# Kernel tuning notes

Measured on AMD Instinct MI355X. Metric: run time of the kernel, lower is better.

The kernel has to match this reference:

```python
import math
import jax, jax.numpy as jnp
import numpy as np

DIM = 1024
HID = 2048  # dim * expansion_factor
QK = 128
G = 256  # group size
NUM_BUCKETS = 32
MAX_DIST = 128
SCALE = QK ** 0.5


def t5_rel_bias(rel_emb, g):
    # non-causal T5 relative position bias over a g x g window
    pos = jnp.arange(g)
    n = pos[:, None] - pos[None, :]  # n = -(k - q) = q - k
    nb = NUM_BUCKETS // 2  # 16
    ret = (n < 0).astype(jnp.int32) * nb
    n = jnp.abs(n)
    max_exact = nb // 2  # 8
    is_small = n < max_exact
    val_large = max_exact + (
        jnp.log(jnp.maximum(n, 1).astype(jnp.float32) / max_exact)
        / math.log(MAX_DIST / max_exact) * (nb - max_exact)
    ).astype(jnp.int32)
    val_large = jnp.minimum(val_large, nb - 1)
    bucket = ret + jnp.where(is_small, n, val_large)
    return rel_emb[bucket, 0] * SCALE  # [g, g]


def setup_inputs() -> dict:
    key = jax.random.key(0)
    ks = jax.random.split(key, 8)
    d = {}
    d['x'] = jax.random.normal(ks[0], (4, 4096, DIM), dtype=jnp.float32)
    d['ln_g'] = jnp.ones((DIM,), jnp.float32)
    d['ln_b'] = jnp.zeros((DIM,), jnp.float32)
    d['W_h'] = jax.random.normal(ks[1], (DIM, 2 * HID), jnp.float32) * (1.0 / math.sqrt(DIM))
    d['b_h'] = jnp.zeros((2 * HID,), jnp.float32)
    d['W_qk'] = jax.random.normal(ks[2], (DIM, QK), jnp.float32) * (1.0 / math.sqrt(DIM))
    d['b_qk'] = jnp.zeros((QK,), jnp.float32)
    d['os_g'] = 1.0 + 0.02 * jax.random.normal(ks[3], (4, QK), jnp.float32)
    d['os_b'] = jnp.zeros((4, QK), jnp.float32)
    d['rel_emb'] = jax.random.normal(ks[4], (NUM_BUCKETS, 1), jnp.float32)
    d['W_o'] = jax.random.normal(ks[5], (HID, DIM), jnp.float32) * (1.0 / math.sqrt(HID))
    d['b_o'] = jnp.zeros((DIM,), jnp.float32)
    return d


def reference(x, ln_g, ln_b, W_h, b_h, W_qk, b_qk, os_g, os_b, rel_emb, W_o, b_o):
    b, n, _ = x.shape
    # LayerNorm
    mu = jnp.mean(x, axis=-1, keepdims=True)
    var = jnp.var(x, axis=-1, keepdims=True)
    normed = (x - mu) * jax.lax.rsqrt(var + 1e-5) * ln_g + ln_b
    # to_hidden -> v, gate ; to_qk
    hidden = jax.nn.silu(normed @ W_h + b_h)  # [b, n, 2*HID]
    v, gate = hidden[..., :HID], hidden[..., HID:]
    qk = jax.nn.silu(normed @ W_qk + b_qk)  # [b, n, QK]
    # offset-scale into 4 heads
    heads = qk[..., None, :] * os_g + os_b  # [b, n, 4, QK]
    quad_q, lin_q, quad_k, lin_k = [heads[..., h, :] for h in range(4)]
    # group: n divisible by G (no padding needed)
    ng = n // G
    grp = lambda t: t.reshape(b, ng, G, -1)
    quad_q, quad_k, lin_q, lin_k, vg = map(grp, (quad_q, quad_k, lin_q, lin_k, v))
    # grouped quadratic attention with ReLU^2 and T5 bias
    sim = jnp.einsum('bgid,bgjd->bgij', quad_q, quad_k) / G
    sim = sim + t5_rel_bias(rel_emb, G)
    attn = jnp.square(jax.nn.relu(sim))
    quad_out = jnp.einsum('bgij,bgjd->bgid', attn, vg)
    # linear attention, reduced over groups (non-causal)
    lin_kv = jnp.einsum('bgnd,bgne->bde', lin_k, vg) / n
    lin_out = jnp.einsum('bgnd,bde->bgne', lin_q, lin_kv)
    out = gate * (quad_out.reshape(b, n, HID) + lin_out.reshape(b, n, HID))
    return out @ W_o + b_o + x
```

## Files before the change

### kernel.cpp

```cpp
#include <hip/hip_runtime.h>
#include <hip/hip_bf16.h>

typedef float  f32x4  __attribute__((ext_vector_type(4)));
typedef __bf16 bf16x8 __attribute__((ext_vector_type(8)));
typedef __bf16 bf16x4 __attribute__((ext_vector_type(4)));

__device__ __forceinline__ float silu_f(float x) { return x / (1.0f + __expf(-x)); }

__device__ __forceinline__ void gload16(const __bf16* g, const char* lds) {
    __builtin_amdgcn_global_load_lds((const __attribute__((address_space(1))) void*)g,
                                     (__attribute__((address_space(3))) void*)lds, 16, 0, 0);
}

__device__ __forceinline__ bf16x8 ds_read16(unsigned addr) {
    bf16x8 d;
    asm volatile("ds_read_b128 %0, %1" : "=v"(d) : "v"(addr));
    return d;
}

template<int IMB>
__device__ __forceinline__ void mfma16(f32x4 (&acc)[8][4], bf16x8 (&bA)[4], bf16x8 (&bB)[4]) {
#pragma unroll
    for (int im = 0; im < 4; ++im)
#pragma unroll
        for (int nj = 0; nj < 4; ++nj)
            acc[IMB + im][nj] = __builtin_amdgcn_mfma_f32_16x16x32_bf16(bA[im], bB[nj], acc[IMB + im][nj], 0, 0, 0);
}

__global__ __launch_bounds__(256) void ln_kernel(const float* __restrict__ x,
                                                 const float* __restrict__ g,
                                                 const float* __restrict__ b,
                                                 __bf16* __restrict__ out) {
    int row = blockIdx.x;
    const float* xr = x + (long)row * 1024;
    int t = threadIdx.x;
    f32x4 v = *(const f32x4*)(xr + t * 4);
    float s  = v[0] + v[1] + v[2] + v[3];
    float ss = v[0]*v[0] + v[1]*v[1] + v[2]*v[2] + v[3]*v[3];
    #pragma unroll
    for (int off = 32; off > 0; off >>= 1) {
        s  += __shfl_down(s, off);
        ss += __shfl_down(ss, off);
    }
    __shared__ float red[8];
    int wave = t >> 6, lane = t & 63;
    if (lane == 0) { red[wave*2] = s; red[wave*2+1] = ss; }
    __syncthreads();
    float S  = red[0] + red[2] + red[4] + red[6];
    float SS = red[1] + red[3] + red[5] + red[7];
    float mean = S * (1.0f/1024.0f);
    float var  = SS * (1.0f/1024.0f) - mean*mean;
    float rstd = rsqrtf(var + 1e-5f);
    __bf16* orow = out + (long)row * 1024;
    #pragma unroll
    for (int j = 0; j < 4; j++) {
        float fv = (v[j] - mean) * rstd * g[t*4+j] + b[t*4+j];
        orow[t*4+j] = (__bf16)fv;
    }
}

__global__ __launch_bounds__(256) void relbias_kernel(const float* __restrict__ rel_emb,
                                                      float* __restrict__ bmat) {
    int idx = blockIdx.x * 256 + threadIdx.x;
    int i = idx >> 8, j = idx & 255;
    int n = i - j;
    int ret = (n < 0) ? 16 : 0;
    int an = (n < 0) ? -n : n;
    int bucket;
    if (an < 8) {
        bucket = ret + an;
    } else {
        float vl = logf((float)an * 0.125f) / 2.772588722239781f * 8.0f;
        int lv = 8 + (int)vl;
        bucket = ret + (lv < 15 ? lv : 15);
    }
    bmat[idx] = rel_emb[bucket] * 11.313708498984761f;
}

__global__ __launch_bounds__(256) void transpose_kernel(const float* __restrict__ in,
                                                        __bf16* __restrict__ out,
                                                        int rows, int cols) {
    __shared__ __bf16 tile[32][33];
    int c0 = blockIdx.x * 32, r0 = blockIdx.y * 32;
    int lx = threadIdx.x, ly = threadIdx.y;
    #pragma unroll
    for (int i = 0; i < 4; i++) {
        int r = ly + i*8;
        tile[r][lx] = (__bf16)in[(long)(r0 + r) * cols + c0 + lx];
    }
    __syncthreads();
    #pragma unroll
    for (int i = 0; i < 4; i++) {
        int c = ly + i*8;
        out[(long)(c0 + c) * rows + r0 + lx] = tile[lx][c];
    }
}

__global__ __launch_bounds__(256) void reduce8_kernel(const __bf16* __restrict__ in,
                                                      __bf16* __restrict__ out) {
    int i = (blockIdx.x * 256 + threadIdx.x) * 4;
    int b = i >> 18;
    int r = i & 262143;
    float s0 = 0.f, s1 = 0.f, s2 = 0.f, s3 = 0.f;
    #pragma unroll
    for (int c = 0; c < 8; ++c) {
        bf16x4 v = *(const bf16x4*)(in + ((long)(b*8 + c) << 18) + r);
        s0 += (float)v[0]; s1 += (float)v[1]; s2 += (float)v[2]; s3 += (float)v[3];
    }
    bf16x4 o; o[0] = (__bf16)s0; o[1] = (__bf16)s1; o[2] = (__bf16)s2; o[3] = (__bf16)s3;
    *(bf16x4*)(out + i) = o;
}

struct G2 {
    const __bf16 *A, *B;
    int lda, ldb, nT;
    float* outF;
    __bf16 *o0, *o1;
    const float *c0, *c1;
};

template<int EPI>
__global__ __launch_bounds__(512, 2) void gemm256(G2 p) {
    __shared__ __align__(128) char smem[131072];
    const int tid = threadIdx.x;
    const int wave = tid >> 6, lane = tid & 63;
    const int wr = (wave >> 2) * 128, wc = (wave & 3) * 64;
    const int lr = lane & 15, kg = lane >> 4;

    const int gx = gridDim.x, gy = gridDim.y;
    int f = blockIdx.y * gx + blockIdx.x;
    int cpx = (gx * gy) >> 3;
    int s8 = (f & 7) * cpx + (f >> 3);
    int bx = s8 / gy, by = s8 % gy;

    const __bf16* gA = p.A + (long)bx * 256 * p.lda;
    const __bf16* gB = p.B + (long)by * 256 * p.ldb;

    const int rS = tid >> 2;
    const int ctb = (tid & 3) * 16;
    const int scol = (ctb ^ ((rS & 3) << 4)) >> 1;

    unsigned lbase = (unsigned)(unsigned long long)(__attribute__((address_space(3))) char*)&smem[0];
    const unsigned swr = ((unsigned)(kg << 4)) ^ ((unsigned)((lr & 3) << 4));
    const unsigned aoffL = (unsigned)((wr + lr) * 64) + swr;
    const unsigned boffL = (unsigned)((wc + lr) * 64) + swr;

    f32x4 acc[8][4] = {};
    bf16x8 bA[4], bB[4];

    auto STAGE = [&](int op, int kh, int st, int slot) {
        const __bf16* gp = op ? gB : gA;
        int ld = op ? p.ldb : p.lda;
        const __bf16* s0 = gp + (long)rS * ld + (long)st * 64 + kh * 32 + scol;
        const char* d = smem + slot * 65536 + op * 32768 + kh * 16384 + (wave << 10);
        gload16(s0, d);
        gload16(s0 + (long)128 * ld, d + 8192);
    };
    auto LDA4 = [&](int slot, int kk, int mb) {
#pragma unroll
        for (int i = 0; i < 4; ++i)
            bA[i] = ds_read16(lbase + slot * 65536 + kk * 16384 + aoffL + (mb + i) * 1024);
    };
    auto LDB4 = [&](int slot, int kk) {
#pragma unroll
        for (int i = 0; i < 4; ++i)
            bB[i] = ds_read16(lbase + slot * 65536 + 32768 + kk * 16384 + boffL + i * 1024);
    };

    STAGE(0, 0, 0, 0); STAGE(1, 0, 0, 0);
    STAGE(0, 1, 0, 0); STAGE(1, 1, 0, 0);
    {
        int t1 = (p.nT > 1) ? 1 : 0;
        STAGE(0, 0, t1, 1); STAGE(1, 0, t1, 1);
    }
    asm volatile("s_waitcnt vmcnt(8)" ::: "memory");
    __builtin_amdgcn_s_barrier();

    for (int s = 0; s < p.nT; ++s) {
        const int db = s & 1;
        const int t1 = (s + 1 < p.nT) ? s + 1 : p.nT - 1;
        const int t2 = (s + 2 < p.nT) ? s + 2 : p.nT - 1;
        const int p1 = (s + 1) & 1;
        LDA4(db, 0, 0); LDB4(db, 0);
        STAGE(0, 1, t1, p1);
        __builtin_amdgcn_s_barrier();
        asm volatile("s_waitcnt lgkmcnt(0)" ::: "memory");
        __builtin_amdgcn_sched_barrier(0);
        __builtin_amdgcn_s_setprio(1);
        mfma16<0>(acc, bA, bB);
        __builtin_amdgcn_s_setprio(0);
        __builtin_amdgcn_s_barrier();
        LDA4(db, 0, 4);
        STAGE(1, 1, t1, p1);
        __builtin_amdgcn_s_barrier();
        asm volatile("s_waitcnt lgkmcnt(0)" ::: "memory");
        __builtin_amdgcn_sched_barrier(0);
        __builtin_amdgcn_s_setprio(1);
        mfma16<4>(acc, bA, bB);
        __builtin_amdgcn_s_setprio(0);
        asm volatile("s_waitcnt vmcnt(8)" ::: "memory");
        __builtin_amdgcn_s_barrier();
        LDA4(db, 1, 0); LDB4(db, 1);
        STAGE(0, 0, t2, db);
        __builtin_amdgcn_s_barrier();
        asm volatile("s_waitcnt lgkmcnt(0)" ::: "memory");
        __builtin_amdgcn_sched_barrier(0);
        __builtin_amdgcn_s_setprio(1);
        mfma16<0>(acc, bA, bB);
        __builtin_amdgcn_s_setprio(0);
        __builtin_amdgcn_s_barrier();
        LDA4(db, 1, 4);
        STAGE(1, 0, t2, db);
        __builtin_amdgcn_s_barrier();
        asm volatile("s_waitcnt lgkmcnt(0)" ::: "memory");
        __builtin_amdgcn_sched_barrier(0);
        __builtin_amdgcn_s_setprio(1);
        mfma16<4>(acc, bA, bB);
        __builtin_amdgcn_s_setprio(0);
        asm volatile("s_waitcnt vmcnt(8)" ::: "memory");
        __builtin_amdgcn_s_barrier();
    }
    asm volatile("s_waitcnt vmcnt(0)" ::: "memory");
    __builtin_amdgcn_s_barrier();

#pragma unroll
    for (int mi = 0; mi < 8; ++mi) {
#pragma unroll
        for (int nj = 0; nj < 4; ++nj) {
            int row0 = bx*256 + wr + mi*16 + kg*4;
            int col  = by*256 + wc + nj*16 + lr;
            if constexpr (EPI == 0) {
                if (col < 2048) {
                    bf16x4 vv;
                    #pragma unroll
                    for (int q = 0; q < 4; q++) vv[q] = (__bf16)silu_f(acc[mi][nj][q] + p.c0[col]);
                    *(bf16x4*)(p.o0 + (long)col*16384 + row0) = vv;
                } else {
                    #pragma unroll
                    for (int q = 0; q < 4; q++)
                        p.o1[(long)(row0+q)*2048 + (col - 2048)] = (__bf16)silu_f(acc[mi][nj][q] + p.c0[col]);
                }
            } else {
                #pragma unroll
                for (int q = 0; q < 4; q++) {
                    long idx = (long)(row0+q)*1024 + col;
                    p.outF[idx] = acc[mi][nj][q] + p.c0[col] + p.c1[idx];
                }
            }
        }
    }
}

struct GP {
    const __bf16* A;
    const __bf16* B;
    const __bf16* A2;
    const __bf16* B2;
    int lda, ldb, kSteps;
    long sAz, sBz, sCz;
    float scale;
    float* outF;
    __bf16 *o0, *o1, *o2, *o3;
    const float *c0, *c1, *c2;
    __bf16* gbuf;
};

template<int EPI>
__global__ __launch_bounds__(256, 2) void gemm_kernel(GP p) {
    __shared__ __bf16 As[128*32];
    __shared__ __bf16 Bs[128*32];
    int z = blockIdx.z;
    const __bf16* A = p.A + (long)z * p.sAz + (long)blockIdx.x * 128 * p.lda;
    const __bf16* B = p.B + (long)z * p.sBz + (long)blockIdx.y * 128 * p.ldb;
    int tid = threadIdx.x;
    int wave = tid >> 6, lane = tid & 63;
    int wr = (wave >> 1) * 64, wc = (wave & 1) * 64;
    int lr = lane & 15, kg = lane >> 4;

    f32x4 acc[4][4] = {};

    int lsub = lane >> 2;
    int scol = (lane & 3) * 8;
    const __bf16* Ag = A + scol + (long)(wave*32 + lsub) * p.lda;
    const __bf16* Bg = B + scol + (long)(wave*32 + lsub) * p.ldb;
    long a16 = (long)16 * p.lda, b16 = (long)16 * p.ldb;
    __bf16* AsW = As + wave * 32 * 32;
    __bf16* BsW = Bs + wave * 32 * 32;

    for (int ks = 0; ks < p.kSteps; ++ks) {
        long k0 = (long)ks * 32;
        __syncthreads();
        gload16(Ag + k0,       (const char*)AsW);
        gload16(Ag + k0 + a16, (const char*)(AsW + 16*32));
        gload16(Bg + k0,       (const char*)BsW);
        gload16(Bg + k0 + b16, (const char*)(BsW + 16*32));
        __syncthreads();
        bf16x8 af[4], bfr[4];
        #pragma unroll
        for (int i = 0; i < 4; i++) af[i]  = *(const bf16x8*)(As + (wr + i*16 + lr)*32 + kg*8);
        #pragma unroll
        for (int i = 0; i < 4; i++) bfr[i] = *(const bf16x8*)(Bs + (wc + i*16 + lr)*32 + kg*8);
        #pragma unroll
        for (int i = 0; i < 4; i++)
            #pragma unroll
            for (int j = 0; j < 4; j++)
                acc[i][j] = __builtin_amdgcn_mfma_f32_16x16x32_bf16(af[i], bfr[j], acc[i][j], 0, 0, 0);
    }

    int bx = blockIdx.x, by = blockIdx.y;
    #pragma unroll
    for (int i = 0; i < 4; i++) {
        #pragma unroll
        for (int j = 0; j < 4; j++) {
            int row0 = bx*128 + wr + i*16 + kg*4;
            int col  = by*128 + wc + j*16 + lr;
            if constexpr (EPI == 1) {
                float sv[4];
                #pragma unroll
                for (int q = 0; q < 4; q++) sv[q] = silu_f(acc[i][j][q] + p.c0[col]);
                #pragma unroll
                for (int q = 0; q < 4; q++) {
                    p.o0[(long)(row0+q)*128 + col] = (__bf16)(sv[q] * p.c1[      col] + p.c2[      col]);
                    p.o1[(long)(row0+q)*128 + col] = (__bf16)(sv[q] * p.c1[256 + col] + p.c2[256 + col]);
                    p.o2[(long)(row0+q)*128 + col] = (__bf16)(sv[q] * p.c1[128 + col] + p.c2[128 + col]);
                }
                bf16x4 lk;
                #pragma unroll
                for (int q = 0; q < 4; q++) lk[q] = (__bf16)(sv[q] * p.c1[384 + col] + p.c2[384 + col]);
                *(bf16x4*)(p.o3 + (long)col*16384 + row0) = lk;
            } else if constexpr (EPI == 2) {
                #pragma unroll
                for (int q = 0; q < 4; q++) {
                    int row = row0 + q;
                    float s = acc[i][j][q] * (1.0f/256.0f) + p.c0[row*256 + col];
                    s = fmaxf(s, 0.0f);
                    p.o0[(long)z*p.sCz + (long)row*256 + col] = (__bf16)(s * s);
                }
            } else if constexpr (EPI == 4) {
                bf16x4 vv;
                #pragma unroll
                for (int q = 0; q < 4; q++) vv[q] = (__bf16)(acc[i][j][q] * p.scale);
                *(bf16x4*)(p.o0 + (long)z*p.sCz + (long)col*128 + row0) = vv;
            } else if constexpr (EPI == 6) {
                #pragma unroll
                for (int q = 0; q < 4; q++) {
                    long idx = (long)(row0+q)*1024 + col;
                    p.outF[idx] = acc[i][j][q] + p.c0[col] + p.c1[idx];
                }
            }
        }
    }
}

__global__ __launch_bounds__(256, 2) void quadlin_kernel(GP p) {
    __shared__ __bf16 As[128*32];
    __shared__ __bf16 Bs[128*32];
    int z = blockIdx.z;
    int batch = z >> 4;
    int tid = threadIdx.x;
    int wave = tid >> 6, lane = tid & 63;
    int wr = (wave >> 1) * 64, wc = (wave & 1) * 64;
    int lr = lane & 15, kg = lane >> 4;
    int lsub = lane >> 2;
    int scol = (lane & 3) * 8;
    __bf16* AsW = As + wave * 32 * 32;
    __bf16* BsW = Bs + wave * 32 * 32;

    f32x4 acc[4][4] = {};

    {
        const __bf16* Ag = p.A + (long)z * 65536 + (long)blockIdx.x * 128 * 256
                         + scol + (long)(wave*32 + lsub) * 256;
        const __bf16* Bg = p.B + (long)z * 256 + (long)blockIdx.y * 128 * 16384
                         + scol + (long)(wave*32 + lsub) * 16384;
        for (int ks = 0; ks < 8; ++ks) {
            long k0 = (long)ks * 32;
            __syncthreads();
            gload16(Ag + k0,             (const char*)AsW);
            gload16(Ag + k0 + 16*256,    (const char*)(AsW + 16*32));
            gload16(Bg + k0,             (const char*)BsW);
            gload16(Bg + k0 + 16L*16384, (const char*)(BsW + 16*32));
            __syncthreads();
            bf16x8 af[4], bfr[4];
            #pragma unroll
            for (int i = 0; i < 4; i++) af[i]  = *(const bf16x8*)(As + (wr + i*16 + lr)*32 + kg*8);
            #pragma unroll
            for (int i = 0; i < 4; i++) bfr[i] = *(const bf16x8*)(Bs + (wc + i*16 + lr)*32 + kg*8);
            #pragma unroll
            for (int i = 0; i < 4; i++)
                #pragma unroll
                for (int j = 0; j < 4; j++)
                    acc[i][j] = __builtin_amdgcn_mfma_f32_16x16x32_bf16(af[i], bfr[j], acc[i][j], 0, 0, 0);
        }
    }
    {
        const __bf16* Ag = p.A2 + ((long)z * 256 + (long)blockIdx.x * 128) * 128
                         + scol + (long)(wave*32 + lsub) * 128;
        const __bf16* Bg = p.B2 + (long)batch * 2048 * 128 + (long)blockIdx.y * 128 * 128
                         + scol + (long)(wave*32 + lsub) * 128;
        for (int ks = 0; ks < 4; ++ks) {
            long k0 = (long)ks * 32;
            __syncthreads();
            gload16(Ag + k0,          (const char*)AsW);
            gload16(Ag + k0 + 16*128, (const char*)(AsW + 16*32));
            gload16(Bg + k0,          (const char*)BsW);
            gload16(Bg + k0 + 16*128, (const char*)(BsW + 16*32));
            __syncthreads();
            bf16x8 af[4], bfr[4];
            #pragma unroll
            for (int i = 0; i < 4; i++) af[i]  = *(const bf16x8*)(As + (wr + i*16 + lr)*32 + kg*8);
            #pragma unroll
            for (int i = 0; i < 4; i++) bfr[i] = *(const bf16x8*)(Bs + (wc + i*16 + lr)*32 + kg*8);
            #pragma unroll
            for (int i = 0; i < 4; i++)
                #pragma unroll
                for (int j = 0; j < 4; j++)
                    acc[i][j] = __builtin_amdgcn_mfma_f32_16x16x32_bf16(af[i], bfr[j], acc[i][j], 0, 0, 0);
        }
    }
    #pragma unroll
    for (int i = 0; i < 4; i++) {
        #pragma unroll
        for (int j = 0; j < 4; j++) {
            int row0 = z*256 + blockIdx.x*128 + wr + i*16 + kg*4;
            int col  = blockIdx.y*128 + wc + j*16 + lr;
            #pragma unroll
            for (int q = 0; q < 4; q++) {
                long idx = (long)(row0+q)*2048 + col;
                float g = (float)p.gbuf[idx];
                p.gbuf[idx] = (__bf16)(g * acc[i][j][q]);
            }
        }
    }
}

extern "C" void kernel_launch(void* const* d_in, const int* in_sizes, int n_in,
                              void* d_out, int out_size, void* d_ws, size_t ws_size,
                              hipStream_t stream) {
    const float* x       = (const float*)d_in[0];
    const float* ln_g    = (const float*)d_in[1];
    const float* ln_b    = (const float*)d_in[2];
    const float* W_h     = (const float*)d_in[3];
    const float* b_h     = (const float*)d_in[4];
    const float* W_qk    = (const float*)d_in[5];
    const float* b_qk    = (const float*)d_in[6];
    const float* os_g    = (const float*)d_in[7];
    const float* os_b    = (const float*)d_in[8];
    const float* rel_emb = (const float*)d_in[9];
    const float* W_o     = (const float*)d_in[10];
    const float* b_o     = (const float*)d_in[11];
    float* out = (float*)d_out;

    const size_t MB = 1024 * 1024;
    if (ws_size < 190 * MB) return;

    char* ws = (char*)d_ws;
    __bf16* gate = (__bf16*)(ws + 0);
    __bf16* vT   = (__bf16*)(ws + 64*MB);
    __bf16* norm = (__bf16*)(ws + 128*MB);
    __bf16* attn = (__bf16*)(ws + 128*MB);
    __bf16* lkvT = (__bf16*)(ws + 136*MB);
    __bf16* lkvP = (__bf16*)(ws + 140*MB);
    __bf16* qq   = (__bf16*)(ws + 160*MB);
    __bf16* qk2  = (__bf16*)(ws + 164*MB);
    __bf16* lq   = (__bf16*)(ws + 168*MB);
    __bf16* lkT  = (__bf16*)(ws + 172*MB);
    float*  bmat = (float* )(ws + 176*MB);
    __bf16* WqkT = (__bf16*)(ws + 176*MB + 256*1024);
    __bf16* WoT  = (__bf16*)(ws + 177*MB);
    __bf16* WhT  = (__bf16*)(ws + 181*MB);

    relbias_kernel<<<256, 256, 0, stream>>>(rel_emb, bmat);
    ln_kernel<<<16384, 256, 0, stream>>>(x, ln_g, ln_b, norm);
    dim3 tb(32, 8);
    transpose_kernel<<<dim3(128, 32), tb, 0, stream>>>(W_h,  WhT,  1024, 4096);
    transpose_kernel<<<dim3(4,   32), tb, 0, stream>>>(W_qk, WqkT, 1024, 128);
    transpose_kernel<<<dim3(32,  64), tb, 0, stream>>>(W_o,  WoT,  2048, 1024);

    {
        G2 p{}; p.A = norm; p.B = WhT; p.lda = 1024; p.ldb = 1024; p.nT = 16;
        p.c0 = b_h; p.o0 = vT; p.o1 = gate;
        gemm256<0><<<dim3(64, 16), 512, 0, stream>>>(p);
    }
    {
        GP p{}; p.A = norm; p.B = WqkT; p.lda = 1024; p.ldb = 1024; p.kSteps = 32;
        p.c0 = b_qk; p.c1 = os_g; p.c2 = os_b;
        p.o0 = qq; p.o1 = qk2; p.o2 = lq; p.o3 = lkT;
        gemm_kernel<1><<<dim3(128, 1, 1), 256, 0, stream>>>(p);
    }
    {
        GP p{}; p.A = qq; p.B = qk2; p.lda = 128; p.ldb = 128; p.kSteps = 4;
        p.sAz = 256*128; p.sBz = 256*128; p.sCz = 256*256;
        p.c0 = bmat; p.o0 = attn;
        gemm_kernel<2><<<dim3(2, 2, 64), 256, 0, stream>>>(p);
    }
    {
        GP p{}; p.A = lkT; p.B = vT; p.lda = 16384; p.ldb = 16384; p.kSteps = 16;
        p.sAz = 512; p.sBz = 512; p.sCz = 2048*128; p.scale = 1.0f/4096.0f;
        p.o0 = lkvP;
        gemm_kernel<4><<<dim3(1, 16, 32), 256, 0, stream>>>(p);
    }
    reduce8_kernel<<<1024, 256, 0, stream>>>(lkvP, lkvT);
    {
        GP p{}; p.A = attn; p.B = vT; p.A2 = lq; p.B2 = lkvT; p.gbuf = gate;
        quadlin_kernel<<<dim3(2, 16, 64), 256, 0, stream>>>(p);
    }
    {
        GP p{}; p.A = gate; p.B = WoT; p.lda = 2048; p.ldb = 2048; p.kSteps = 64;
        p.c0 = b_o; p.c1 = x; p.outF = out;
        gemm_kernel<6><<<dim3(128, 8, 1), 256, 0, stream>>>(p);
    }
}
```

Baseline: 473.5 us.

## Halve K-tile in 256x256 hidden GEMM to cut LDS and restructure pipeline

Rewrites the main hidden-projection GEMM to use 32-wide K tiles instead of 64. This halves shared memory to 64KB and raises the launch-bounds occupancy hint from 2 to 4. The loop now reads all A and B fragments for a tile up front and splits the MFMA work into two halves around a single staging point, replacing four barrier-separated phases with fewer barriers per tile. It trades more loop iterations and more frequent global loads for higher occupancy and less synchronization, though 512 threads with a 256x256 accumulator may still limit how many blocks can actually share a CU.

```diff
diff --git a/kernel.cpp b/kernel.cpp
--- a/kernel.cpp
+++ b/kernel.cpp
@@ -16,15 +16,6 @@
     bf16x8 d;
     asm volatile("ds_read_b128 %0, %1" : "=v"(d) : "v"(addr));
     return d;
-}
-
-template<int IMB>
-__device__ __forceinline__ void mfma16(f32x4 (&acc)[8][4], bf16x8 (&bA)[4], bf16x8 (&bB)[4]) {
-#pragma unroll
-    for (int im = 0; im < 4; ++im)
-#pragma unroll
-        for (int nj = 0; nj < 4; ++nj)
-            acc[IMB + im][nj] = __builtin_amdgcn_mfma_f32_16x16x32_bf16(bA[im], bB[nj], acc[IMB + im][nj], 0, 0, 0);
 }
 
 __global__ __launch_bounds__(256) void ln_kernel(const float* __restrict__ x,
@@ -120,8 +111,8 @@
 };
 
 template<int EPI>
-__global__ __launch_bounds__(512, 2) void gemm256(G2 p) {
-    __shared__ __align__(128) char smem[131072];
+__global__ __launch_bounds__(512, 4) void gemm256v2(G2 p) {
+    __shared__ __align__(128) char smem[65536];
     const int tid = threadIdx.x;
     const int wave = tid >> 6, lane = tid & 63;
     const int wr = (wave >> 2) * 128, wc = (wave & 3) * 64;
@@ -143,81 +134,60 @@
     unsigned lbase = (unsigned)(unsigned long long)(__attribute__((address_space(3))) char*)&smem[0];
     const unsigned swr = ((unsigned)(kg << 4)) ^ ((unsigned)((lr & 3) << 4));
     const unsigned aoffL = (unsigned)((wr + lr) * 64) + swr;
-    const unsigned boffL = (unsigned)((wc + lr) * 64) + swr;
+    const unsigned boffL = (unsigned)((wc + lr) * 64) + swr + 16384u;
 
     f32x4 acc[8][4] = {};
-    bf16x8 bA[4], bB[4];
-
-    auto STAGE = [&](int op, int kh, int st, int slot) {
+    bf16x8 bA[4], bA2[4], bB[4];
+
+    auto STAGE = [&](int op, int st, int slot) {
         const __bf16* gp = op ? gB : gA;
         int ld = op ? p.ldb : p.lda;
-        const __bf16* s0 = gp + (long)rS * ld + (long)st * 64 + kh * 32 + scol;
-        const char* d = smem + slot * 65536 + op * 32768 + kh * 16384 + (wave << 10);
+        const __bf16* s0 = gp + (long)rS * ld + (long)st * 32 + scol;
+        const char* d = smem + slot * 32768 + op * 16384 + (wave << 10);
         gload16(s0, d);
         gload16(s0 + (long)128 * ld, d + 8192);
     };
-    auto LDA4 = [&](int slot, int kk, int mb) {
+
+    {
+        int t1 = (p.nT > 1) ? 1 : 0;
+        STAGE(0, 0, 0); STAGE(1, 0, 0);
+        STAGE(0, t1, 1); STAGE(1, t1, 1);
+    }
+    asm volatile("s_waitcnt vmcnt(4)" ::: "memory");
+    __builtin_amdgcn_s_barrier();
+
+    const int nT = p.nT;
+    for (int t = 0; t < nT; ++t) {
+        const int db = t & 1;
+        const int t2 = (t + 2 < nT) ? t + 2 : nT - 1;
+        const unsigned sb = (unsigned)(db * 32768);
+#pragma unroll
+        for (int i = 0; i < 4; ++i) bA[i]  = ds_read16(lbase + sb + aoffL + i * 1024);
+#pragma unroll
+        for (int i = 0; i < 4; ++i) bB[i]  = ds_read16(lbase + sb + boffL + i * 1024);
+#pragma unroll
+        for (int i = 0; i < 4; ++i) bA2[i] = ds_read16(lbase + sb + aoffL + (4 + i) * 1024);
+        asm volatile("s_waitcnt lgkmcnt(4)" ::: "memory");
+        __builtin_amdgcn_sched_barrier(0);
+        __builtin_amdgcn_s_setprio(1);
 #pragma unroll
         for (int i = 0; i < 4; ++i)
-            bA[i] = ds_read16(lbase + slot * 65536 + kk * 16384 + aoffL + (mb + i) * 1024);
-    };
-    auto LDB4 = [&](int slot, int kk) {
-#pragma unroll
-        for (int i = 0; i < 4; ++i)
-            bB[i] = ds_read16(lbase + slot * 65536 + 32768 + kk * 16384 + boffL + i * 1024);
-    };
-
-    STAGE(0, 0, 0, 0); STAGE(1, 0, 0, 0);
-    STAGE(0, 1, 0, 0); STAGE(1, 1, 0, 0);
-    {
-        int t1 = (p.nT > 1) ? 1 : 0;
-        STAGE(0, 0, t1, 1); STAGE(1, 0, t1, 1);
-    }
-    asm volatile("s_waitcnt vmcnt(8)" ::: "memory");
-    __builtin_amdgcn_s_barrier();
-
-    for (int s = 0; s < p.nT; ++s) {
-        const int db = s & 1;
-        const int t1 = (s + 1 < p.nT) ? s + 1 : p.nT - 1;
-        const int t2 = (s + 2 < p.nT) ? s + 2 : p.nT - 1;
-        const int p1 = (s + 1) & 1;
-        LDA4(db, 0, 0); LDB4(db, 0);
-        STAGE(0, 1, t1, p1);
-        __builtin_amdgcn_s_barrier();
+#pragma unroll
+            for (int j = 0; j < 4; ++j)
+                acc[i][j] = __builtin_amdgcn_mfma_f32_16x16x32_bf16(bA[i], bB[j], acc[i][j], 0, 0, 0);
+        __builtin_amdgcn_s_setprio(0);
         asm volatile("s_waitcnt lgkmcnt(0)" ::: "memory");
         __builtin_amdgcn_sched_barrier(0);
+        __builtin_amdgcn_s_barrier();
+        STAGE(0, t2, db); STAGE(1, t2, db);
         __builtin_amdgcn_s_setprio(1);
-        mfma16<0>(acc, bA, bB);
+#pragma unroll
+        for (int i = 0; i < 4; ++i)
+#pragma unroll
+            for (int j = 0; j < 4; ++j)
+                acc[4 + i][j] = __builtin_amdgcn_mfma_f32_16x16x32_bf16(bA2[i], bB[j], acc[4 + i][j], 0, 0, 0);
         __builtin_amdgcn_s_setprio(0);
-        __builtin_amdgcn_s_barrier();
-        LDA4(db, 0, 4);
-        STAGE(1, 1, t1, p1);
-        __builtin_amdgcn_s_barrier();
-        asm volatile("s_waitcnt lgkmcnt(0)" ::: "memory");
-        __builtin_amdgcn_sched_barrier(0);
-        __builtin_amdgcn_s_setprio(1);
-        mfma16<4>(acc, bA, bB);
-        __builtin_amdgcn_s_setprio(0);
-        asm volatile("s_waitcnt vmcnt(8)" ::: "memory");
-        __builtin_amdgcn_s_barrier();
-        LDA4(db, 1, 0); LDB4(db, 1);
-        STAGE(0, 0, t2, db);
-        __builtin_amdgcn_s_barrier();
-        asm volatile("s_waitcnt lgkmcnt(0)" ::: "memory");
-        __builtin_amdgcn_sched_barrier(0);
-        __builtin_amdgcn_s_setprio(1);
-        mfma16<0>(acc, bA, bB);
-        __builtin_amdgcn_s_setprio(0);
-        __builtin_amdgcn_s_barrier();
-        LDA4(db, 1, 4);
-        STAGE(1, 0, t2, db);
-        __builtin_amdgcn_s_barrier();
-        asm volatile("s_waitcnt lgkmcnt(0)" ::: "memory");
-        __builtin_amdgcn_sched_barrier(0);
-        __builtin_amdgcn_s_setprio(1);
-        mfma16<4>(acc, bA, bB);
-        __builtin_amdgcn_s_setprio(0);
-        asm volatile("s_waitcnt vmcnt(8)" ::: "memory");
+        asm volatile("s_waitcnt vmcnt(4)" ::: "memory");
         __builtin_amdgcn_s_barrier();
     }
     asm volatile("s_waitcnt vmcnt(0)" ::: "memory");
@@ -478,9 +448,9 @@
     transpose_kernel<<<dim3(32,  64), tb, 0, stream>>>(W_o,  WoT,  2048, 1024);
 
     {
-        G2 p{}; p.A = norm; p.B = WhT; p.lda = 1024; p.ldb = 1024; p.nT = 16;
+        G2 p{}; p.A = norm; p.B = WhT; p.lda = 1024; p.ldb = 1024; p.nT = 32;
         p.c0 = b_h; p.o0 = vT; p.o1 = gate;
-        gemm256<0><<<dim3(64, 16), 512, 0, stream>>>(p);
+        gemm256v2<0><<<dim3(64, 16), 512, 0, stream>>>(p);
     }
     {
         GP p{}; p.A = norm; p.B = WqkT; p.lda = 1024; p.ldb = 1024; p.kSteps = 32;
```

Result: slower. 1.609 ms (+239.8%).
